# Kernel optimization log

Hardware: AMD Instinct MI355X
Metric: run time of the kernel (lower is better)

## Reference

```python
import jax, jax.numpy as jnp
import numpy as np

EMB = 1024
HEAD = 64

def setup_inputs() -> dict:
    key = jax.random.key(0)
    kx, kq, kk, kv = jax.random.split(key, 4)
    x = jax.random.normal(kx, (8, 2048, EMB), dtype=jnp.float32)
    # nn.Linear(emb, head, bias=False): y = x @ W.T, W: [head, emb]. Store as [emb, head].
    s = 1.0 / np.sqrt(EMB)
    Wq = jax.random.uniform(kq, (EMB, HEAD), jnp.float32, -s, s)
    Wk = jax.random.uniform(kk, (EMB, HEAD), jnp.float32, -s, s)
    Wv = jax.random.uniform(kv, (EMB, HEAD), jnp.float32, -s, s)
    return {"x": x, "Wq": Wq, "Wk": Wk, "Wv": Wv}

def reference(x, Wq, Wk, Wv):
    B, T, C = x.shape
    q = x @ Wq  # [B,T,H]
    k = x @ Wk
    v = x @ Wv
    # NOTE: original scales by emb_size C, not head_size.
    wei = jnp.einsum('bth,bsh->bts', q, k) / jnp.sqrt(jnp.asarray(C, x.dtype))
    causal = jnp.tril(jnp.ones((T, T), dtype=bool))
    wei = jnp.where(causal, wei, -jnp.inf)
    wei = jax.nn.softmax(wei, axis=-1)
    return jnp.einsum('bts,bsh->bth', wei, v)
```

## Files before the change

kernel.cpp:

```cpp
#include <hip/hip_runtime.h>
#include <hip/hip_bf16.h>

typedef __bf16 bf16_t;
typedef __bf16 bf16x8 __attribute__((ext_vector_type(8)));
typedef __bf16 bf16x4 __attribute__((ext_vector_type(4)));
typedef float  f32x4  __attribute__((ext_vector_type(4)));

#define MFMA_BF16(A, B, C) __builtin_amdgcn_mfma_f32_16x16x32_bf16((A), (B), (C), 0, 0, 0)

#define BATCH 8
#define SEQ   2048
#define EMB   1024
#define HEAD  64

typedef __attribute__((address_space(3))) void as3_void;
typedef const __attribute__((address_space(1))) void as1_void;
#define GLOAD_LDS16(g, l) \
  __builtin_amdgcn_global_load_lds((as1_void*)(g), (as3_void*)(l), 16, 0, 0)

__global__ __launch_bounds__(256) void wtrans_kernel(
    const float* __restrict__ Wq, const float* __restrict__ Wk,
    const float* __restrict__ Wv, bf16_t* __restrict__ WT)
{
  __shared__ float tile[64][65];
  const int m  = blockIdx.x >> 4;
  const int kt = blockIdx.x & 15;
  const float* W = (m == 0) ? Wq : (m == 1) ? Wk : Wv;
  const float scale = (m == 0) ? 0.045084219f : 1.0f;
  const int k0 = kt * 64;

  #pragma unroll
  for (int i = 0; i < 16; ++i) {
    int idx = i * 256 + threadIdx.x;
    int kk = idx >> 6, n = idx & 63;
    tile[kk][n] = W[(size_t)(k0 + kk) * HEAD + n];
  }
  __syncthreads();
  #pragma unroll
  for (int i = 0; i < 16; ++i) {
    int idx = i * 256 + threadIdx.x;
    int n = idx >> 6, kk = idx & 63;
    WT[((size_t)m * HEAD + n) * EMB + k0 + kk] = (bf16_t)(tile[kk][n] * scale);
  }
}

#define A_BYTES 16384
#define B_BYTES 24576
#define BUF_BYTES 40960

__global__ __launch_bounds__(512, 1) void qkv_kernel(
    const float* __restrict__ x, const bf16_t* __restrict__ WT,
    bf16_t* __restrict__ qo, bf16_t* __restrict__ ko, bf16_t* __restrict__ vT)
{
  __shared__ char lds[4 * BUF_BYTES];

  const int tid  = threadIdx.x;
  const int lane = tid & 63;
  const int wave = tid >> 6;
  const int l15 = lane & 15, l4 = lane >> 4;
  const int wm = wave >> 2, wn = wave & 3;
  const int rowbase = blockIdx.x * 64;
  const int phase = (blockIdx.x >> 3) & 15;

  const int a_rsub = lane >> 4;
  const int b_rsub = lane >> 3;
  const int b_koff = ((lane & 7) * 16) ^ (b_rsub << 4);

  const int aswz = (l15 & 7) << 5;
  const int bswz = (l15 & 7) << 4;

  f32x4 acc[2][3];
  #pragma unroll
  for (int m = 0; m < 2; ++m)
    #pragma unroll
    for (int n = 0; n < 3; ++n) acc[m][n] = (f32x4){0.f, 0.f, 0.f, 0.f};

#define STAGE(t)                                                               \
  {                                                                            \
    char* buf = lds + ((t) & 3) * BUF_BYTES;                                   \
    const int tp = ((t) + phase) & 15;                                         \
    _Pragma("unroll")                                                          \
    for (int j = 0; j < 2; ++j) {                                              \
      const int g = 2 * wave + j;                                              \
      const int koff = (l15 * 16) ^ ((((j) << 2) | a_rsub) << 5);              \
      const char* src = (const char*)x + (size_t)(rowbase + 4 * g + a_rsub)    \
                        * 4096 + (size_t)tp * 256 + koff;                      \
      GLOAD_LDS16(src, buf + g * 1024);                                        \
    }                                                                          \
    _Pragma("unroll")                                                          \
    for (int j = 0; j < 3; ++j) {                                              \
      const int g = 3 * wave + j;                                              \
      const char* src = (const char*)WT + (size_t)(8 * g + b_rsub) * 2048      \
                        + (size_t)tp * 128 + b_koff;                           \
      GLOAD_LDS16(src, buf + A_BYTES + g * 1024);                              \
    }                                                                          \
  }

#define COMPUTE(t)                                                             \
  {                                                                            \
    const char* Ab = lds + ((t) & 3) * BUF_BYTES;                              \
    const char* Bb = Ab + A_BYTES;                                             \
    _Pragma("unroll")                                                          \
    for (int ks = 0; ks < 2; ++ks) {                                           \
      bf16x8 afr[2];                                                           \
      _Pragma("unroll")                                                        \
      for (int m = 0; m < 2; ++m) {                                            \
        const int R = wm * 32 + m * 16 + l15;                                  \
        const char* rp = Ab + R * 256 + ((ks * 128 + l4 * 32) ^ aswz);         \
        f32x4 p0 = *(const f32x4*)(rp);                                        \
        f32x4 p1 = *(const f32x4*)(rp + 16);                                   \
        bf16x8 a;                                                              \
        a[0] = (bf16_t)p0.x; a[1] = (bf16_t)p0.y;                              \
        a[2] = (bf16_t)p0.z; a[3] = (bf16_t)p0.w;                              \
        a[4] = (bf16_t)p1.x; a[5] = (bf16_t)p1.y;                              \
        a[6] = (bf16_t)p1.z; a[7] = (bf16_t)p1.w;                              \
        afr[m] = a;                                                            \
      }                                                                        \
      _Pragma("unroll")                                                        \
      for (int n = 0; n < 3; ++n) {                                            \
        const int Rb = wn * 48 + n * 16 + l15;                                 \
        bf16x8 b = *(const bf16x8*)(Bb + Rb * 128 + ((ks * 64 + l4 * 16) ^ bswz)); \
        acc[0][n] = MFMA_BF16(afr[0], b, acc[0][n]);                           \
        acc[1][n] = MFMA_BF16(afr[1], b, acc[1][n]);                           \
      }                                                                        \
    }                                                                          \
  }

  STAGE(0); STAGE(1); STAGE(2);
  asm volatile("s_waitcnt vmcnt(10)" ::: "memory");
  __builtin_amdgcn_s_barrier();

  for (int t = 0; t < 13; ++t) {
    COMPUTE(t);
    STAGE(t + 3);
    asm volatile("s_waitcnt vmcnt(10)" ::: "memory");
    __builtin_amdgcn_s_barrier();
  }
  COMPUTE(13);
  asm volatile("s_waitcnt vmcnt(5)" ::: "memory");
  __builtin_amdgcn_s_barrier();
  COMPUTE(14);
  asm volatile("s_waitcnt vmcnt(0)" ::: "memory");
  __builtin_amdgcn_s_barrier();
  COMPUTE(15);
#undef STAGE
#undef COMPUTE

  #pragma unroll
  for (int n = 0; n < 3; ++n) {
    const int col = wn * 48 + n * 16;
    #pragma unroll
    for (int m = 0; m < 2; ++m) {
      const int r0 = rowbase + wm * 32 + m * 16 + l4 * 4;
      if (col < 64) {
        #pragma unroll
        for (int i = 0; i < 4; ++i)
          qo[(size_t)(r0 + i) * HEAD + col + l15] = (bf16_t)acc[m][n][i];
      } else if (col < 128) {
        #pragma unroll
        for (int i = 0; i < 4; ++i)
          ko[(size_t)(r0 + i) * HEAD + col - 64 + l15] = (bf16_t)acc[m][n][i];
      } else {
        const int h = col - 128 + l15;
        bf16x4 pk;
        #pragma unroll
        for (int i = 0; i < 4; ++i) pk[i] = (bf16_t)acc[m][n][i];
        *(bf16x4*)(vT + ((size_t)(r0 >> 11) * HEAD + h) * SEQ + (r0 & 2047)) = pk;
      }
    }
  }
}

__global__ __launch_bounds__(256) void attn_kernel(
    const bf16_t* __restrict__ q, const bf16_t* __restrict__ k,
    const bf16_t* __restrict__ vT, float* __restrict__ out)
{
  __shared__ bf16_t P[4][16][72];
  __shared__ float olds[4][16][68];
  __shared__ float lsums[4][16];
  const int lane = threadIdx.x & 63;
  const int wave = threadIdx.x >> 6;
  const int l15 = lane & 15, l4 = lane >> 4;
  const int batch = blockIdx.x & 7;
  const int u = 63 - (int)(blockIdx.x >> 3);
  const int qrowA = u * 32;
  const int qrowB = u * 32 + 16;
  const int ntiles = (u >> 1) + 1;

  const bf16_t* kb = k  + (size_t)batch * SEQ * HEAD;
  const bf16_t* vb = vT + (size_t)batch * HEAD * SEQ;
  const bf16_t* qbA = q + ((size_t)batch * SEQ + qrowA) * HEAD;
  const bf16_t* qbB = q + ((size_t)batch * SEQ + qrowB) * HEAD;

  const bf16x8 aqA0 = *(const bf16x8*)(qbA + (size_t)l15 * HEAD + l4 * 8);
  const bf16x8 aqA1 = *(const bf16x8*)(qbA + (size_t)l15 * HEAD + 32 + l4 * 8);
  const bf16x8 aqB0 = *(const bf16x8*)(qbB + (size_t)l15 * HEAD + l4 * 8);
  const bf16x8 aqB1 = *(const bf16x8*)(qbB + (size_t)l15 * HEAD + 32 + l4 * 8);

  f32x4 oA[4], oB[4];
  #pragma unroll
  for (int i = 0; i < 4; ++i) {
    oA[i] = (f32x4){0.f, 0.f, 0.f, 0.f};
    oB[i] = (f32x4){0.f, 0.f, 0.f, 0.f};
  }
  float lsA[4] = {0.f, 0.f, 0.f, 0.f};
  float lsB[4] = {0.f, 0.f, 0.f, 0.f};

  for (int t = wave; t < ntiles; t += 4) {
    const int kv0 = t * 64;

    f32x4 sA[4], sB[4];
    #pragma unroll
    for (int nf = 0; nf < 4; ++nf) {
      sA[nf] = (f32x4){0.f, 0.f, 0.f, 0.f};
      sB[nf] = (f32x4){0.f, 0.f, 0.f, 0.f};
    }
    __builtin_amdgcn_s_setprio(1);
    #pragma unroll
    for (int nf = 0; nf < 4; ++nf) {
      const bf16_t* kp = kb + (size_t)(kv0 + nf * 16 + l15) * HEAD + l4 * 8;
      bf16x8 b0 = *(const bf16x8*)kp;
      bf16x8 b1 = *(const bf16x8*)(kp + 32);
      sA[nf] = MFMA_BF16(aqA0, b0, sA[nf]);
      sB[nf] = MFMA_BF16(aqB0, b0, sB[nf]);
      sA[nf] = MFMA_BF16(aqA1, b1, sA[nf]);
      sB[nf] = MFMA_BF16(aqB1, b1, sB[nf]);
    }
    __builtin_amdgcn_s_setprio(0);

    bf16x8 v0[4], v1[4];
    #pragma unroll
    for (int nf = 0; nf < 4; ++nf) {
      const bf16_t* vp = vb + (size_t)(nf * 16 + l15) * SEQ + kv0 + l4 * 8;
      v0[nf] = *(const bf16x8*)vp;
      v1[nf] = *(const bf16x8*)(vp + 32);
    }

    const bool diag = (t == ntiles - 1);

    {
      float tsum[4] = {0.f, 0.f, 0.f, 0.f};
      #pragma unroll
      for (int nf = 0; nf < 4; ++nf) {
        #pragma unroll
        for (int i2 = 0; i2 < 4; ++i2) {
          float e = exp2f(sA[nf][i2]);
          if (diag) {
            const int col = kv0 + nf * 16 + l15;
            const int row = qrowA + l4 * 4 + i2;
            e = (col <= row) ? e : 0.f;
          }
          tsum[i2] += e;
          P[wave][l4 * 4 + i2][nf * 16 + l15] = (bf16_t)e;
        }
      }
      bf16x8 ap0 = *(const bf16x8*)&P[wave][l15][l4 * 8];
      bf16x8 ap1 = *(const bf16x8*)&P[wave][l15][32 + l4 * 8];
      __builtin_amdgcn_s_setprio(1);
      #pragma unroll
      for (int nf = 0; nf < 4; ++nf) {
        oA[nf] = MFMA_BF16(ap0, v0[nf], oA[nf]);
        oA[nf] = MFMA_BF16(ap1, v1[nf], oA[nf]);
      }
      __builtin_amdgcn_s_setprio(0);
      #pragma unroll
      for (int i2 = 0; i2 < 4; ++i2) lsA[i2] += tsum[i2];
    }

    {
      float tsum[4] = {0.f, 0.f, 0.f, 0.f};
      #pragma unroll
      for (int nf = 0; nf < 4; ++nf) {
        #pragma unroll
        for (int i2 = 0; i2 < 4; ++i2) {
          float e = exp2f(sB[nf][i2]);
          if (diag) {
            const int col = kv0 + nf * 16 + l15;
            const int row = qrowB + l4 * 4 + i2;
            e = (col <= row) ? e : 0.f;
          }
          tsum[i2] += e;
          P[wave][l4 * 4 + i2][nf * 16 + l15] = (bf16_t)e;
        }
      }
      bf16x8 ap0 = *(const bf16x8*)&P[wave][l15][l4 * 8];
      bf16x8 ap1 = *(const bf16x8*)&P[wave][l15][32 + l4 * 8];
      __builtin_amdgcn_s_setprio(1);
      #pragma unroll
      for (int nf = 0; nf < 4; ++nf) {
        oB[nf] = MFMA_BF16(ap0, v0[nf], oB[nf]);
        oB[nf] = MFMA_BF16(ap1, v1[nf], oB[nf]);
      }
      __builtin_amdgcn_s_setprio(0);
      #pragma unroll
      for (int i2 = 0; i2 < 4; ++i2) lsB[i2] += tsum[i2];
    }
  }

  #pragma unroll
  for (int pass = 0; pass < 2; ++pass) {
    #pragma unroll
    for (int i = 0; i < 4; ++i) {
      float v = pass == 0 ? lsA[i] : lsB[i];
      v += __shfl_xor(v, 1);
      v += __shfl_xor(v, 2);
      v += __shfl_xor(v, 4);
      v += __shfl_xor(v, 8);
      if (l15 == 0) lsums[wave][l4 * 4 + i] = v;
    }
    #pragma unroll
    for (int nf = 0; nf < 4; ++nf)
      #pragma unroll
      for (int i = 0; i < 4; ++i)
        olds[wave][l4 * 4 + i][nf * 16 + l15] = pass == 0 ? oA[nf][i] : oB[nf][i];
    __syncthreads();

    {
      const int r = threadIdx.x >> 4, c0 = threadIdx.x & 15;
      const float sum = lsums[0][r] + lsums[1][r] + lsums[2][r] + lsums[3][r];
      const float rinv = 1.0f / sum;
      const int qrow = pass == 0 ? qrowA : qrowB;
      float* ob = out + ((size_t)batch * SEQ + qrow + r) * HEAD;
      #pragma unroll
      for (int j = 0; j < 4; ++j) {
        const int c = c0 + 16 * j;
        float v = olds[0][r][c] + olds[1][r][c] + olds[2][r][c] + olds[3][r][c];
        ob[c] = v * rinv;
      }
    }
    __syncthreads();
  }
}

extern "C" void kernel_launch(void* const* d_in, const int* in_sizes, int n_in,
                              void* d_out, int out_size, void* d_ws, size_t ws_size,
                              hipStream_t stream)
{
  const float* x  = (const float*)d_in[0];
  const float* Wq = (const float*)d_in[1];
  const float* Wk = (const float*)d_in[2];
  const float* Wv = (const float*)d_in[3];
  float* out = (float*)d_out;

  const size_t SZ_QKV = (size_t)BATCH * SEQ * HEAD * sizeof(bf16_t);
  if (ws_size < 3 * SZ_QKV + (size_t)192 * EMB * sizeof(bf16_t)) return;
  char* ws = (char*)d_ws;
  bf16_t* qo = (bf16_t*)(ws);
  bf16_t* ko = (bf16_t*)(ws + SZ_QKV);
  bf16_t* vT = (bf16_t*)(ws + 2 * SZ_QKV);
  bf16_t* WT = (bf16_t*)(ws + 3 * SZ_QKV);

  wtrans_kernel<<<dim3(48),  dim3(256), 0, stream>>>(Wq, Wk, Wv, WT);
  qkv_kernel  <<<dim3(256), dim3(512), 0, stream>>>(x, WT, qo, ko, vT);
  attn_kernel <<<dim3(512), dim3(256), 0, stream>>>(qo, ko, vT, out);
}
```

Measured before the change: 51.03 us.

## Load x directly to registers in QKV GEMM and overlap softmax with V loads

The QKV projection kernel no longer stages fp32 x tiles through LDS with global_load_lds. Each lane now loads its A fragments straight into a triple-buffered register array two steps ahead, and only the weight tiles stay in the LDS ring. This cuts LDS size and LDS read traffic but raises register pressure. In the attention kernel, both halves' exp/mask work now runs around the V loads using separate P buffers, so the V latency can hide behind the exponentials. The block-to-query-tile order is also changed to mix heavy and light causal tiles.

```diff
diff --git a/kernel.cpp b/kernel.cpp
--- a/kernel.cpp
+++ b/kernel.cpp
@@ -44,15 +44,13 @@
   }
 }
 
-#define A_BYTES 16384
 #define B_BYTES 24576
-#define BUF_BYTES 40960
 
 __global__ __launch_bounds__(512, 1) void qkv_kernel(
     const float* __restrict__ x, const bf16_t* __restrict__ WT,
     bf16_t* __restrict__ qo, bf16_t* __restrict__ ko, bf16_t* __restrict__ vT)
 {
-  __shared__ char lds[4 * BUF_BYTES];
+  __shared__ char lds[4 * B_BYTES];
 
   const int tid  = threadIdx.x;
   const int lane = tid & 63;
@@ -62,53 +60,55 @@
   const int rowbase = blockIdx.x * 64;
   const int phase = (blockIdx.x >> 3) & 15;
 
-  const int a_rsub = lane >> 4;
   const int b_rsub = lane >> 3;
   const int b_koff = ((lane & 7) * 16) ^ (b_rsub << 4);
-
-  const int aswz = (l15 & 7) << 5;
   const int bswz = (l15 & 7) << 4;
 
+  const float* xrow0 = x + (size_t)(rowbase + wm * 32 + l15) * EMB;
+
+  float4 as0[8], as1[8], as2[8];
   f32x4 acc[2][3];
   #pragma unroll
   for (int m = 0; m < 2; ++m)
     #pragma unroll
     for (int n = 0; n < 3; ++n) acc[m][n] = (f32x4){0.f, 0.f, 0.f, 0.f};
 
-#define STAGE(t)                                                               \
+#define B_STAGE(t)                                                             \
   {                                                                            \
-    char* buf = lds + ((t) & 3) * BUF_BYTES;                                   \
+    char* buf = lds + ((t) & 3) * B_BYTES;                                     \
     const int tp = ((t) + phase) & 15;                                         \
-    _Pragma("unroll")                                                          \
-    for (int j = 0; j < 2; ++j) {                                              \
-      const int g = 2 * wave + j;                                              \
-      const int koff = (l15 * 16) ^ ((((j) << 2) | a_rsub) << 5);              \
-      const char* src = (const char*)x + (size_t)(rowbase + 4 * g + a_rsub)    \
-                        * 4096 + (size_t)tp * 256 + koff;                      \
-      GLOAD_LDS16(src, buf + g * 1024);                                        \
-    }                                                                          \
     _Pragma("unroll")                                                          \
     for (int j = 0; j < 3; ++j) {                                              \
       const int g = 3 * wave + j;                                              \
       const char* src = (const char*)WT + (size_t)(8 * g + b_rsub) * 2048      \
                         + (size_t)tp * 128 + b_koff;                           \
-      GLOAD_LDS16(src, buf + A_BYTES + g * 1024);                              \
+      GLOAD_LDS16(src, buf + g * 1024);                                        \
     }                                                                          \
   }
 
-#define COMPUTE(t)                                                             \
+#define A_ISSUE(s, ARR)                                                        \
   {                                                                            \
-    const char* Ab = lds + ((t) & 3) * BUF_BYTES;                              \
-    const char* Bb = Ab + A_BYTES;                                             \
+    const int tp = ((s) + phase) & 15;                                         \
+    _Pragma("unroll")                                                          \
+    for (int m = 0; m < 2; ++m)                                                \
+      _Pragma("unroll")                                                        \
+      for (int ks = 0; ks < 2; ++ks)                                           \
+        _Pragma("unroll")                                                      \
+        for (int h = 0; h < 2; ++h)                                            \
+          ARR[m * 4 + ks * 2 + h] = *(const float4*)(xrow0 + m * 16 * EMB      \
+                                     + tp * 64 + ks * 32 + l4 * 8 + h * 4);    \
+  }
+
+#define COMPUTE(t, ARR)                                                        \
+  {                                                                            \
+    const char* Bb = lds + ((t) & 3) * B_BYTES;                                \
     _Pragma("unroll")                                                          \
     for (int ks = 0; ks < 2; ++ks) {                                           \
       bf16x8 afr[2];                                                           \
       _Pragma("unroll")                                                        \
       for (int m = 0; m < 2; ++m) {                                            \
-        const int R = wm * 32 + m * 16 + l15;                                  \
-        const char* rp = Ab + R * 256 + ((ks * 128 + l4 * 32) ^ aswz);         \
-        f32x4 p0 = *(const f32x4*)(rp);                                        \
-        f32x4 p1 = *(const f32x4*)(rp + 16);                                   \
+        float4 p0 = ARR[m * 4 + ks * 2 + 0];                                   \
+        float4 p1 = ARR[m * 4 + ks * 2 + 1];                                   \
         bf16x8 a;                                                              \
         a[0] = (bf16_t)p0.x; a[1] = (bf16_t)p0.y;                              \
         a[2] = (bf16_t)p0.z; a[3] = (bf16_t)p0.w;                              \
@@ -126,25 +126,43 @@
     }                                                                          \
   }
 
-  STAGE(0); STAGE(1); STAGE(2);
-  asm volatile("s_waitcnt vmcnt(10)" ::: "memory");
+#define ITER(t, AU, AF, VM)                                                    \
+  COMPUTE(t, AU);                                                              \
+  A_ISSUE((t) + 2, AF);                                                        \
+  B_STAGE((t) + 3);                                                            \
+  asm volatile("s_waitcnt vmcnt(" #VM ")" ::: "memory");                       \
   __builtin_amdgcn_s_barrier();
 
-  for (int t = 0; t < 13; ++t) {
-    COMPUTE(t);
-    STAGE(t + 3);
-    asm volatile("s_waitcnt vmcnt(10)" ::: "memory");
-    __builtin_amdgcn_s_barrier();
-  }
-  COMPUTE(13);
-  asm volatile("s_waitcnt vmcnt(5)" ::: "memory");
+  B_STAGE(0); B_STAGE(1); B_STAGE(2);
+  A_ISSUE(0, as0); A_ISSUE(1, as1);
+  asm volatile("s_waitcnt vmcnt(8)" ::: "memory");
   __builtin_amdgcn_s_barrier();
-  COMPUTE(14);
+
+  ITER(0,  as0, as2, 11)
+  ITER(1,  as1, as0, 14)
+  ITER(2,  as2, as1, 14)
+  ITER(3,  as0, as2, 14)
+  ITER(4,  as1, as0, 14)
+  ITER(5,  as2, as1, 14)
+  ITER(6,  as0, as2, 14)
+  ITER(7,  as1, as0, 14)
+  ITER(8,  as2, as1, 14)
+  ITER(9,  as0, as2, 14)
+  ITER(10, as1, as0, 14)
+  ITER(11, as2, as1, 14)
+  ITER(12, as0, as2, 14)
+  COMPUTE(13, as1);
+  A_ISSUE(15, as0);
+  asm volatile("s_waitcnt vmcnt(11)" ::: "memory");
+  __builtin_amdgcn_s_barrier();
+  COMPUTE(14, as2);
   asm volatile("s_waitcnt vmcnt(0)" ::: "memory");
   __builtin_amdgcn_s_barrier();
-  COMPUTE(15);
-#undef STAGE
+  COMPUTE(15, as0);
+#undef ITER
 #undef COMPUTE
+#undef A_ISSUE
+#undef B_STAGE
 
   #pragma unroll
   for (int n = 0; n < 3; ++n) {
@@ -175,14 +193,15 @@
     const bf16_t* __restrict__ q, const bf16_t* __restrict__ k,
     const bf16_t* __restrict__ vT, float* __restrict__ out)
 {
-  __shared__ bf16_t P[4][16][72];
+  __shared__ bf16_t P[4][2][16][72];
   __shared__ float olds[4][16][68];
   __shared__ float lsums[4][16];
   const int lane = threadIdx.x & 63;
   const int wave = threadIdx.x >> 6;
   const int l15 = lane & 15, l4 = lane >> 4;
   const int batch = blockIdx.x & 7;
-  const int u = 63 - (int)(blockIdx.x >> 3);
+  const int idx = (int)(blockIdx.x >> 3);
+  const int u = (blockIdx.x < 256) ? idx : (95 - idx);
   const int qrowA = u * 32;
   const int qrowB = u * 32 + 16;
   const int ntiles = (u >> 1) + 1;
@@ -208,6 +227,7 @@
 
   for (int t = wave; t < ntiles; t += 4) {
     const int kv0 = t * 64;
+    const bool diag = (t == ntiles - 1);
 
     f32x4 sA[4], sB[4];
     #pragma unroll
@@ -228,6 +248,22 @@
     }
     __builtin_amdgcn_s_setprio(0);
 
+    float tsA[4] = {0.f, 0.f, 0.f, 0.f};
+    #pragma unroll
+    for (int nf = 0; nf < 4; ++nf) {
+      #pragma unroll
+      for (int i2 = 0; i2 < 4; ++i2) {
+        float e = exp2f(sA[nf][i2]);
+        if (diag) {
+          const int col = kv0 + nf * 16 + l15;
+          const int row = qrowA + l4 * 4 + i2;
+          e = (col <= row) ? e : 0.f;
+        }
+        tsA[i2] += e;
+        P[wave][0][l4 * 4 + i2][nf * 16 + l15] = (bf16_t)e;
+      }
+    }
+
     bf16x8 v0[4], v1[4];
     #pragma unroll
     for (int nf = 0; nf < 4; ++nf) {
@@ -236,26 +272,25 @@
       v1[nf] = *(const bf16x8*)(vp + 32);
     }
 
-    const bool diag = (t == ntiles - 1);
+    float tsB[4] = {0.f, 0.f, 0.f, 0.f};
+    #pragma unroll
+    for (int nf = 0; nf < 4; ++nf) {
+      #pragma unroll
+      for (int i2 = 0; i2 < 4; ++i2) {
+        float e = exp2f(sB[nf][i2]);
+        if (diag) {
+          const int col = kv0 + nf * 16 + l15;
+          const int row = qrowB + l4 * 4 + i2;
+          e = (col <= row) ? e : 0.f;
+        }
+        tsB[i2] += e;
+        P[wave][1][l4 * 4 + i2][nf * 16 + l15] = (bf16_t)e;
+      }
+    }
 
     {
-      float tsum[4] = {0.f, 0.f, 0.f, 0.f};
-      #pragma unroll
-      for (int nf = 0; nf < 4; ++nf) {
-        #pragma unroll
-        for (int i2 = 0; i2 < 4; ++i2) {
-          float e = exp2f(sA[nf][i2]);
-          if (diag) {
-            const int col = kv0 + nf * 16 + l15;
-            const int row = qrowA + l4 * 4 + i2;
-            e = (col <= row) ? e : 0.f;
-          }
-          tsum[i2] += e;
-          P[wave][l4 * 4 + i2][nf * 16 + l15] = (bf16_t)e;
-        }
-      }
-      bf16x8 ap0 = *(const bf16x8*)&P[wave][l15][l4 * 8];
-      bf16x8 ap1 = *(const bf16x8*)&P[wave][l15][32 + l4 * 8];
+      bf16x8 ap0 = *(const bf16x8*)&P[wave][0][l15][l4 * 8];
+      bf16x8 ap1 = *(const bf16x8*)&P[wave][0][l15][32 + l4 * 8];
       __builtin_amdgcn_s_setprio(1);
       #pragma unroll
       for (int nf = 0; nf < 4; ++nf) {
@@ -264,36 +299,20 @@
       }
       __builtin_amdgcn_s_setprio(0);
       #pragma unroll
-      for (int i2 = 0; i2 < 4; ++i2) lsA[i2] += tsum[i2];
-    }
-
+      for (int i2 = 0; i2 < 4; ++i2) lsA[i2] += tsA[i2];
+    }
     {
-      float tsum[4] = {0.f, 0.f, 0.f, 0.f};
+      bf16x8 bp0 = *(const bf16x8*)&P[wave][1][l15][l4 * 8];
+      bf16x8 bp1 = *(const bf16x8*)&P[wave][1][l15][32 + l4 * 8];
+      __builtin_amdgcn_s_setprio(1);
       #pragma unroll
       for (int nf = 0; nf < 4; ++nf) {
-        #pragma unroll
-        for (int i2 = 0; i2 < 4; ++i2) {
-          float e = exp2f(sB[nf][i2]);
-          if (diag) {
-            const int col = kv0 + nf * 16 + l15;
-            const int row = qrowB + l4 * 4 + i2;
-            e = (col <= row) ? e : 0.f;
-          }
-          tsum[i2] += e;
-          P[wave][l4 * 4 + i2][nf * 16 + l15] = (bf16_t)e;
-        }
-      }
-      bf16x8 ap0 = *(const bf16x8*)&P[wave][l15][l4 * 8];
-      bf16x8 ap1 = *(const bf16x8*)&P[wave][l15][32 + l4 * 8];
-      __builtin_amdgcn_s_setprio(1);
-      #pragma unroll
-      for (int nf = 0; nf < 4; ++nf) {
-        oB[nf] = MFMA_BF16(ap0, v0[nf], oB[nf]);
-        oB[nf] = MFMA_BF16(ap1, v1[nf], oB[nf]);
+        oB[nf] = MFMA_BF16(bp0, v0[nf], oB[nf]);
+        oB[nf] = MFMA_BF16(bp1, v1[nf], oB[nf]);
       }
       __builtin_amdgcn_s_setprio(0);
       #pragma unroll
-      for (int i2 = 0; i2 < 4; ++i2) lsB[i2] += tsum[i2];
+      for (int i2 = 0; i2 < 4; ++i2) lsB[i2] += tsB[i2];
     }
   }
 
```

Result: slower. 69.12 us (+35.4%).

## Double-buffer P and reorder softmax before V loads; change block-to-tile mapping

Applied to the files above, without the earlier changes.

The P staging buffer gets a separate slot for each of the A and B query halves. Both exponentials are now computed before either PV matmul, with the first softmax issued before the V loads, so exp work can overlap the V fetch latency and the LDS round-trip. The block-to-query-tile mapping also changes: the first 256 blocks take tiles in ascending order and the rest in descending order, which alters load balance across the grid. The second P buffer doubles LDS use for P, which could affect occupancy.

```diff
diff --git a/kernel.cpp b/kernel.cpp
--- a/kernel.cpp
+++ b/kernel.cpp
@@ -175,14 +175,15 @@
     const bf16_t* __restrict__ q, const bf16_t* __restrict__ k,
     const bf16_t* __restrict__ vT, float* __restrict__ out)
 {
-  __shared__ bf16_t P[4][16][72];
+  __shared__ bf16_t P[4][2][16][72];
   __shared__ float olds[4][16][68];
   __shared__ float lsums[4][16];
   const int lane = threadIdx.x & 63;
   const int wave = threadIdx.x >> 6;
   const int l15 = lane & 15, l4 = lane >> 4;
   const int batch = blockIdx.x & 7;
-  const int u = 63 - (int)(blockIdx.x >> 3);
+  const int idx = (int)(blockIdx.x >> 3);
+  const int u = (blockIdx.x < 256) ? idx : (95 - idx);
   const int qrowA = u * 32;
   const int qrowB = u * 32 + 16;
   const int ntiles = (u >> 1) + 1;
@@ -208,6 +209,7 @@
 
   for (int t = wave; t < ntiles; t += 4) {
     const int kv0 = t * 64;
+    const bool diag = (t == ntiles - 1);
 
     f32x4 sA[4], sB[4];
     #pragma unroll
@@ -228,6 +230,22 @@
     }
     __builtin_amdgcn_s_setprio(0);
 
+    float tsA[4] = {0.f, 0.f, 0.f, 0.f};
+    #pragma unroll
+    for (int nf = 0; nf < 4; ++nf) {
+      #pragma unroll
+      for (int i2 = 0; i2 < 4; ++i2) {
+        float e = exp2f(sA[nf][i2]);
+        if (diag) {
+          const int col = kv0 + nf * 16 + l15;
+          const int row = qrowA + l4 * 4 + i2;
+          e = (col <= row) ? e : 0.f;
+        }
+        tsA[i2] += e;
+        P[wave][0][l4 * 4 + i2][nf * 16 + l15] = (bf16_t)e;
+      }
+    }
+
     bf16x8 v0[4], v1[4];
     #pragma unroll
     for (int nf = 0; nf < 4; ++nf) {
@@ -236,26 +254,25 @@
       v1[nf] = *(const bf16x8*)(vp + 32);
     }
 
-    const bool diag = (t == ntiles - 1);
+    float tsB[4] = {0.f, 0.f, 0.f, 0.f};
+    #pragma unroll
+    for (int nf = 0; nf < 4; ++nf) {
+      #pragma unroll
+      for (int i2 = 0; i2 < 4; ++i2) {
+        float e = exp2f(sB[nf][i2]);
+        if (diag) {
+          const int col = kv0 + nf * 16 + l15;
+          const int row = qrowB + l4 * 4 + i2;
+          e = (col <= row) ? e : 0.f;
+        }
+        tsB[i2] += e;
+        P[wave][1][l4 * 4 + i2][nf * 16 + l15] = (bf16_t)e;
+      }
+    }
 
     {
-      float tsum[4] = {0.f, 0.f, 0.f, 0.f};
-      #pragma unroll
-      for (int nf = 0; nf < 4; ++nf) {
-        #pragma unroll
-        for (int i2 = 0; i2 < 4; ++i2) {
-          float e = exp2f(sA[nf][i2]);
-          if (diag) {
-            const int col = kv0 + nf * 16 + l15;
-            const int row = qrowA + l4 * 4 + i2;
-            e = (col <= row) ? e : 0.f;
-          }
-          tsum[i2] += e;
-          P[wave][l4 * 4 + i2][nf * 16 + l15] = (bf16_t)e;
-        }
-      }
-      bf16x8 ap0 = *(const bf16x8*)&P[wave][l15][l4 * 8];
-      bf16x8 ap1 = *(const bf16x8*)&P[wave][l15][32 + l4 * 8];
+      bf16x8 ap0 = *(const bf16x8*)&P[wave][0][l15][l4 * 8];
+      bf16x8 ap1 = *(const bf16x8*)&P[wave][0][l15][32 + l4 * 8];
       __builtin_amdgcn_s_setprio(1);
       #pragma unroll
       for (int nf = 0; nf < 4; ++nf) {
@@ -264,36 +281,20 @@
       }
       __builtin_amdgcn_s_setprio(0);
       #pragma unroll
-      for (int i2 = 0; i2 < 4; ++i2) lsA[i2] += tsum[i2];
-    }
-
+      for (int i2 = 0; i2 < 4; ++i2) lsA[i2] += tsA[i2];
+    }
     {
-      float tsum[4] = {0.f, 0.f, 0.f, 0.f};
+      bf16x8 bp0 = *(const bf16x8*)&P[wave][1][l15][l4 * 8];
+      bf16x8 bp1 = *(const bf16x8*)&P[wave][1][l15][32 + l4 * 8];
+      __builtin_amdgcn_s_setprio(1);
       #pragma unroll
       for (int nf = 0; nf < 4; ++nf) {
-        #pragma unroll
-        for (int i2 = 0; i2 < 4; ++i2) {
-          float e = exp2f(sB[nf][i2]);
-          if (diag) {
-            const int col = kv0 + nf * 16 + l15;
-            const int row = qrowB + l4 * 4 + i2;
-            e = (col <= row) ? e : 0.f;
-          }
-          tsum[i2] += e;
-          P[wave][l4 * 4 + i2][nf * 16 + l15] = (bf16_t)e;
-        }
-      }
-      bf16x8 ap0 = *(const bf16x8*)&P[wave][l15][l4 * 8];
-      bf16x8 ap1 = *(const bf16x8*)&P[wave][l15][32 + l4 * 8];
-      __builtin_amdgcn_s_setprio(1);
-      #pragma unroll
-      for (int nf = 0; nf < 4; ++nf) {
-        oB[nf] = MFMA_BF16(ap0, v0[nf], oB[nf]);
-        oB[nf] = MFMA_BF16(ap1, v1[nf], oB[nf]);
+        oB[nf] = MFMA_BF16(bp0, v0[nf], oB[nf]);
+        oB[nf] = MFMA_BF16(bp1, v1[nf], oB[nf]);
       }
       __builtin_amdgcn_s_setprio(0);
       #pragma unroll
-      for (int i2 = 0; i2 < 4; ++i2) lsB[i2] += tsum[i2];
+      for (int i2 = 0; i2 < 4; ++i2) lsB[i2] += tsB[i2];
     }
   }
 
```

After: 48.24 us (median of 2 runs). 5.5% less time.
